# Kernel optimization log

Measured on AMD Instinct MI355X. Metric: run time of the kernel, lower is better.

The kernel has to match this reference:

```python
import jax, jax.numpy as jnp
import numpy as np


def setup_inputs() -> dict:
    key = jax.random.key(0)
    kx, ky = jax.random.split(key)
    N, D = 8192, 128
    x = jax.random.normal(kx, (N, D), dtype=jnp.float32)
    y = jax.random.normal(ky, (N, D), dtype=jnp.float32)
    return {"x": x, "y": y}


def reference(x, y):
    # L2 contrastive loss (Kostic et al. 2024, NCP):
    #   1/(N(N-1)) * sum_{i != j} <x_i, y_j>^2  -  2/N * sum_i <x_i, y_i>
    N = x.shape[0]
    K = x @ y.T                      # (N, N) pairwise dot products
    diag = jnp.diagonal(K)           # <x_i, y_i>
    off_diag_sq = jnp.sum(K * K) - jnp.sum(diag * diag)
    loss = off_diag_sq / (N * (N - 1)) - 2.0 / N * jnp.sum(diag)
    return loss
```

## Files before the change

kernel.cpp:

```cpp
#include <hip/hip_runtime.h>

#define DD 128
#define SR 72
#define PP 128
#define NB (2*PP)
#define NT 36
#define DOTB 144

typedef float f32x4 __attribute__((ext_vector_type(4)));
typedef short s16x8 __attribute__((ext_vector_type(8)));

__global__ __launch_bounds__(512)
void gram_kernel(const float* __restrict__ x, const float* __restrict__ y,
                 float* __restrict__ apart, float* __restrict__ bpart,
                 double* __restrict__ ds1, double* __restrict__ ds2,
                 float* __restrict__ out, int N)
{
  const int blk = blockIdx.x;
  const bool isX = blk < PP;
  const int p = isX ? blk : blk - PP;
  const float* __restrict__ src = isX ? x : y;
  const int slab = N / PP;
  const int row0 = p * slab;

  __shared__ __align__(16) unsigned short sh_hi[DD * SR];
  __shared__ __align__(16) unsigned short sh_lo[DD * SR];
  __shared__ double wred[8][2];

  const int tid = threadIdx.x;
  const int wave = tid >> 6, lane = tid & 63;
  const int rloc = tid >> 3;
  const int fg = tid & 7;

  if (blk == 0 && tid == 0) out[0] = 0.0f;

  const int start = (9 * wave) >> 1;
  const int cnt = 4 + (wave & 1);
  int tr_[5], tc_[5];
#pragma unroll
  for (int j = 0; j < 5; ++j) {
    const int tile = start + j;
    int r = 0;
#pragma unroll
    for (int q = 1; q < 8; ++q) r += (tile >= ((q * (17 - q)) >> 1)) ? 1 : 0;
    tr_[j] = r;
    tc_[j] = tile - ((r * (17 - r)) >> 1) + r;
  }

  f32x4 acc[5];
#pragma unroll
  for (int t = 0; t < 5; ++t)
#pragma unroll
    for (int k = 0; k < 4; ++k) acc[t][k] = 0.f;

  double s1 = 0.0, s2 = 0.0;

  {
    const float* cb = src + (size_t)row0 * DD;
    const float4* rowp = (const float4*)(cb + rloc * DD);
    float4 v0 = rowp[fg], v1 = rowp[fg + 8], v2 = rowp[fg + 16], v3 = rowp[fg + 24];

    if (isX) {
      const float4* yrp = (const float4*)(y + (size_t)row0 * DD + rloc * DD);
      float4 w0 = yrp[fg], w1 = yrp[fg + 8], w2 = yrp[fg + 16], w3 = yrp[fg + 24];
      float d = v0.x*w0.x + v0.y*w0.y + v0.z*w0.z + v0.w*w0.w
              + v1.x*w1.x + v1.y*w1.y + v1.z*w1.z + v1.w*w1.w
              + v2.x*w2.x + v2.y*w2.y + v2.z*w2.z + v2.w*w2.w
              + v3.x*w3.x + v3.y*w3.y + v3.z*w3.z + v3.w*w3.w;
      d += __shfl_down(d, 4, 8);
      d += __shfl_down(d, 2, 8);
      d += __shfl_down(d, 1, 8);
      if (fg == 0) { s1 += (double)d; s2 += (double)d * (double)d; }
    }

    {
      float vals[16] = {v0.x, v0.y, v0.z, v0.w, v1.x, v1.y, v1.z, v1.w,
                        v2.x, v2.y, v2.z, v2.w, v3.x, v3.y, v3.z, v3.w};
#pragma unroll
      for (int j = 0; j < 4; ++j)
#pragma unroll
        for (int cc = 0; cc < 4; ++cc) {
          const int m = ((fg + (j << 3)) << 2) + cc;
          const float vv = vals[j * 4 + cc];
          const unsigned int b = __float_as_uint(vv);
          const unsigned short hb = (unsigned short)(b >> 16);
          const float hf = __uint_as_float(b & 0xffff0000u);
          const float lf = vv - hf;
          const unsigned short lb = (unsigned short)(__float_as_uint(lf) >> 16);
          sh_hi[m * SR + rloc] = hb;
          sh_lo[m * SR + rloc] = lb;
        }
    }
    __syncthreads();

#pragma unroll
    for (int j = 0; j < 5; ++j) {
      if (j < cnt) {
        const int ar0 = (tr_[j] * 16 + (lane & 15)) * SR;
        const int br0 = (tc_[j] * 16 + (lane & 15)) * SR;
#pragma unroll
        for (int kb = 0; kb < 64; kb += 32) {
          const int ko = kb + ((lane >> 4) << 3);
          const s16x8 ahi = *(const s16x8*)&sh_hi[ar0 + ko];
          const s16x8 alo = *(const s16x8*)&sh_lo[ar0 + ko];
          const s16x8 bhi = *(const s16x8*)&sh_hi[br0 + ko];
          const s16x8 blo = *(const s16x8*)&sh_lo[br0 + ko];
          acc[j] = __builtin_amdgcn_mfma_f32_16x16x32_bf16(ahi, bhi, acc[j], 0, 0, 0);
          acc[j] = __builtin_amdgcn_mfma_f32_16x16x32_bf16(ahi, blo, acc[j], 0, 0, 0);
          acc[j] = __builtin_amdgcn_mfma_f32_16x16x32_bf16(alo, bhi, acc[j], 0, 0, 0);
        }
      }
    }
  }

  f32x4* __restrict__ dst4 = (f32x4*)(isX ? apart : bpart) + (size_t)p * (NT * 64);
#pragma unroll
  for (int j = 0; j < 5; ++j)
    if (j < cnt) dst4[(start + j) * 64 + lane] = acc[j];

  if (isX) {
    s1 += __shfl_down(s1, 32, 64); s2 += __shfl_down(s2, 32, 64);
    s1 += __shfl_down(s1, 16, 64); s2 += __shfl_down(s2, 16, 64);
    s1 += __shfl_down(s1, 8, 64);  s2 += __shfl_down(s2, 8, 64);
    if (lane == 0) { wred[wave][0] = s1; wred[wave][1] = s2; }
    __syncthreads();
    if (tid == 0) {
      double t1 = 0.0, t2 = 0.0;
#pragma unroll
      for (int g = 0; g < 8; ++g) { t1 += wred[g][0]; t2 += wred[g][1]; }
      ds1[p] = t1;
      ds2[p] = t2;
    }
  }
}

__global__ __launch_bounds__(256)
void dotfin_kernel(const float* __restrict__ apart, const float* __restrict__ bpart,
                   const double* __restrict__ ds1, const double* __restrict__ ds2,
                   float* __restrict__ out, int N)
{
  __shared__ f32x4 sA[16][16], sB[16][16];
  __shared__ double red[4][2];

  const int blk = blockIdx.x;
  const int tid = threadIdx.x;
  const double invNN1 = 1.0 / ((double)N * (double)(N - 1));

  if (blk < DOTB) {
    const int s = tid & 15;
    const int pg = tid >> 4;
    const f32x4* a4 = (const f32x4*)apart;
    const f32x4* b4 = (const f32x4*)bpart;
    const int base = blk * 16 + s;

    f32x4 sa = {0.f, 0.f, 0.f, 0.f}, sb = {0.f, 0.f, 0.f, 0.f};
#pragma unroll
    for (int i = 0; i < 8; ++i) {
      const int p = pg + (i << 4);
      sa += a4[(size_t)p * (NT * 64) + base];
      sb += b4[(size_t)p * (NT * 64) + base];
    }

    sA[pg][s] = sa;
    sB[pg][s] = sb;
    __syncthreads();

    if (tid < 16) {
      f32x4 ta = sA[0][tid], tb = sB[0][tid];
#pragma unroll
      for (int g = 1; g < 16; ++g) { ta += sA[g][tid]; tb += sB[g][tid]; }
      const int tile = (blk * 16 + tid) >> 6;
      const double w = ((0xA44208101ULL >> tile) & 1) ? 1.0 : 2.0;
      double pr = w * ((double)ta[0] * (double)tb[0]
                     + (double)ta[1] * (double)tb[1]
                     + (double)ta[2] * (double)tb[2]
                     + (double)ta[3] * (double)tb[3]);
      pr += __shfl_down(pr, 8, 16);
      pr += __shfl_down(pr, 4, 16);
      pr += __shfl_down(pr, 2, 16);
      pr += __shfl_down(pr, 1, 16);
      if (tid == 0) atomicAdd(out, (float)(pr * invNN1));
    }
  } else {
    const int wv = tid >> 6, lane = tid & 63;
    double t1 = (tid < PP) ? ds1[tid] : 0.0;
    double t2 = (tid < PP) ? ds2[tid] : 0.0;
#pragma unroll
    for (int off = 32; off > 0; off >>= 1) {
      t1 += __shfl_down(t1, off, 64);
      t2 += __shfl_down(t2, off, 64);
    }
    if (lane == 0) { red[wv][0] = t1; red[wv][1] = t2; }
    __syncthreads();
    if (tid == 0) {
      double d1 = red[0][0] + red[1][0] + red[2][0] + red[3][0];
      double d2 = red[0][1] + red[1][1] + red[2][1] + red[3][1];
      atomicAdd(out, (float)(-d2 * invNN1 - (2.0 / N) * d1));
    }
  }
}

extern "C" void kernel_launch(void* const* d_in, const int* in_sizes, int n_in,
                              void* d_out, int out_size, void* d_ws, size_t ws_size,
                              hipStream_t stream) {
  const float* x = (const float*)d_in[0];
  const float* y = (const float*)d_in[1];
  float* out = (float*)d_out;
  const int N = in_sizes[0] / DD;

  char* w = (char*)d_ws;
  float* apart = (float*)w;                              w += (size_t)PP * NT * 256 * 4;
  float* bpart = (float*)w;                              w += (size_t)PP * NT * 256 * 4;
  double* ds1  = (double*)w;                             w += PP * 8;
  double* ds2  = (double*)w;                             w += PP * 8;

  gram_kernel<<<NB, 512, 0, stream>>>(x, y, apart, bpart, ds1, ds2, out, N);
  dotfin_kernel<<<DOTB + 1, 256, 0, stream>>>(apart, bpart, ds1, ds2, out, N);
}
```

Before: 68.81 us.

## Split Gram tile work across twice as many blocks and widen finalize grid

The gram kernel now launches 512 blocks instead of 256. Each slab's 36 upper-triangular 16x16 Gram tiles are split into two halves of 18, and each block computes only one half. This gives each wave 2-3 tiles instead of 4-5 and improves CU coverage on a 256-CU part. The cost is that every slab is loaded and split into bf16 hi/lo twice. The dot/finalize kernel doubles its block count, with each block handling 8 float4 lanes over 32 partition groups to shorten the per-block reduction.

```diff
diff --git a/kernel.cpp b/kernel.cpp
--- a/kernel.cpp
+++ b/kernel.cpp
@@ -3,9 +3,9 @@
 #define DD 128
 #define SR 72
 #define PP 128
-#define NB (2*PP)
+#define GB 512
 #define NT 36
-#define DOTB 144
+#define DOTB 288
 
 typedef float f32x4 __attribute__((ext_vector_type(4)));
 typedef short s16x8 __attribute__((ext_vector_type(8)));
@@ -16,12 +16,15 @@
                  double* __restrict__ ds1, double* __restrict__ ds2,
                  float* __restrict__ out, int N)
 {
-  const int blk = blockIdx.x;
-  const bool isX = blk < PP;
-  const int p = isX ? blk : blk - PP;
+  const int b = blockIdx.x;
+  const int half = b >> 8;
+  const int inner = b & 255;
+  const bool isX = inner < PP;
+  const int p = inner & (PP - 1);
   const float* __restrict__ src = isX ? x : y;
   const int slab = N / PP;
   const int row0 = p * slab;
+  const bool doDiag = isX && (half == 0);
 
   __shared__ __align__(16) unsigned short sh_hi[DD * SR];
   __shared__ __align__(16) unsigned short sh_lo[DD * SR];
@@ -32,14 +35,14 @@
   const int rloc = tid >> 3;
   const int fg = tid & 7;
 
-  if (blk == 0 && tid == 0) out[0] = 0.0f;
-
-  const int start = (9 * wave) >> 1;
-  const int cnt = 4 + (wave & 1);
-  int tr_[5], tc_[5];
-#pragma unroll
-  for (int j = 0; j < 5; ++j) {
-    const int tile = start + j;
+  if (b == 0 && tid == 0) out[0] = 0.0f;
+
+  const int start = 2 * wave + (wave == 7 ? 1 : 0);
+  const int cnt = (wave >= 6) ? 3 : 2;
+  int tr_[3], tc_[3];
+#pragma unroll
+  for (int j = 0; j < 3; ++j) {
+    const int tile = 18 * half + start + j;
     int r = 0;
 #pragma unroll
     for (int q = 1; q < 8; ++q) r += (tile >= ((q * (17 - q)) >> 1)) ? 1 : 0;
@@ -47,9 +50,9 @@
     tc_[j] = tile - ((r * (17 - r)) >> 1) + r;
   }
 
-  f32x4 acc[5];
-#pragma unroll
-  for (int t = 0; t < 5; ++t)
+  f32x4 acc[3];
+#pragma unroll
+  for (int t = 0; t < 3; ++t)
 #pragma unroll
     for (int k = 0; k < 4; ++k) acc[t][k] = 0.f;
 
@@ -60,7 +63,7 @@
     const float4* rowp = (const float4*)(cb + rloc * DD);
     float4 v0 = rowp[fg], v1 = rowp[fg + 8], v2 = rowp[fg + 16], v3 = rowp[fg + 24];
 
-    if (isX) {
+    if (doDiag) {
       const float4* yrp = (const float4*)(y + (size_t)row0 * DD + rloc * DD);
       float4 w0 = yrp[fg], w1 = yrp[fg + 8], w2 = yrp[fg + 16], w3 = yrp[fg + 24];
       float d = v0.x*w0.x + v0.y*w0.y + v0.z*w0.z + v0.w*w0.w
@@ -82,9 +85,9 @@
         for (int cc = 0; cc < 4; ++cc) {
           const int m = ((fg + (j << 3)) << 2) + cc;
           const float vv = vals[j * 4 + cc];
-          const unsigned int b = __float_as_uint(vv);
-          const unsigned short hb = (unsigned short)(b >> 16);
-          const float hf = __uint_as_float(b & 0xffff0000u);
+          const unsigned int bb = __float_as_uint(vv);
+          const unsigned short hb = (unsigned short)(bb >> 16);
+          const float hf = __uint_as_float(bb & 0xffff0000u);
           const float lf = vv - hf;
           const unsigned short lb = (unsigned short)(__float_as_uint(lf) >> 16);
           sh_hi[m * SR + rloc] = hb;
@@ -94,7 +97,7 @@
     __syncthreads();
 
 #pragma unroll
-    for (int j = 0; j < 5; ++j) {
+    for (int j = 0; j < 3; ++j) {
       if (j < cnt) {
         const int ar0 = (tr_[j] * 16 + (lane & 15)) * SR;
         const int br0 = (tc_[j] * 16 + (lane & 15)) * SR;
@@ -115,14 +118,16 @@
 
   f32x4* __restrict__ dst4 = (f32x4*)(isX ? apart : bpart) + (size_t)p * (NT * 64);
 #pragma unroll
-  for (int j = 0; j < 5; ++j)
-    if (j < cnt) dst4[(start + j) * 64 + lane] = acc[j];
-
-  if (isX) {
+  for (int j = 0; j < 3; ++j)
+    if (j < cnt) dst4[(18 * half + start + j) * 64 + lane] = acc[j];
+
+  if (doDiag) {
     s1 += __shfl_down(s1, 32, 64); s2 += __shfl_down(s2, 32, 64);
     s1 += __shfl_down(s1, 16, 64); s2 += __shfl_down(s2, 16, 64);
     s1 += __shfl_down(s1, 8, 64);  s2 += __shfl_down(s2, 8, 64);
     if (lane == 0) { wred[wave][0] = s1; wred[wave][1] = s2; }
+  }
+  if (doDiag) {
     __syncthreads();
     if (tid == 0) {
       double t1 = 0.0, t2 = 0.0;
@@ -139,7 +144,7 @@
                    const double* __restrict__ ds1, const double* __restrict__ ds2,
                    float* __restrict__ out, int N)
 {
-  __shared__ f32x4 sA[16][16], sB[16][16];
+  __shared__ f32x4 sA[32][9], sB[32][9];
   __shared__ double red[4][2];
 
   const int blk = blockIdx.x;
@@ -147,16 +152,16 @@
   const double invNN1 = 1.0 / ((double)N * (double)(N - 1));
 
   if (blk < DOTB) {
-    const int s = tid & 15;
-    const int pg = tid >> 4;
+    const int s = tid & 7;
+    const int pg = tid >> 3;
     const f32x4* a4 = (const f32x4*)apart;
     const f32x4* b4 = (const f32x4*)bpart;
-    const int base = blk * 16 + s;
+    const int base = blk * 8 + s;
 
     f32x4 sa = {0.f, 0.f, 0.f, 0.f}, sb = {0.f, 0.f, 0.f, 0.f};
 #pragma unroll
-    for (int i = 0; i < 8; ++i) {
-      const int p = pg + (i << 4);
+    for (int i = 0; i < 4; ++i) {
+      const int p = pg + (i << 5);
       sa += a4[(size_t)p * (NT * 64) + base];
       sb += b4[(size_t)p * (NT * 64) + base];
     }
@@ -165,20 +170,19 @@
     sB[pg][s] = sb;
     __syncthreads();
 
-    if (tid < 16) {
+    if (tid < 8) {
       f32x4 ta = sA[0][tid], tb = sB[0][tid];
 #pragma unroll
-      for (int g = 1; g < 16; ++g) { ta += sA[g][tid]; tb += sB[g][tid]; }
-      const int tile = (blk * 16 + tid) >> 6;
+      for (int g = 1; g < 32; ++g) { ta += sA[g][tid]; tb += sB[g][tid]; }
+      const int tile = (blk * 8 + tid) >> 6;
       const double w = ((0xA44208101ULL >> tile) & 1) ? 1.0 : 2.0;
       double pr = w * ((double)ta[0] * (double)tb[0]
                      + (double)ta[1] * (double)tb[1]
                      + (double)ta[2] * (double)tb[2]
                      + (double)ta[3] * (double)tb[3]);
-      pr += __shfl_down(pr, 8, 16);
-      pr += __shfl_down(pr, 4, 16);
-      pr += __shfl_down(pr, 2, 16);
-      pr += __shfl_down(pr, 1, 16);
+      pr += __shfl_down(pr, 4, 8);
+      pr += __shfl_down(pr, 2, 8);
+      pr += __shfl_down(pr, 1, 8);
       if (tid == 0) atomicAdd(out, (float)(pr * invNN1));
     }
   } else {
@@ -214,6 +218,6 @@
   double* ds1  = (double*)w;                             w += PP * 8;
   double* ds2  = (double*)w;                             w += PP * 8;
 
-  gram_kernel<<<NB, 512, 0, stream>>>(x, y, apart, bpart, ds1, ds2, out, N);
+  gram_kernel<<<GB, 512, 0, stream>>>(x, y, apart, bpart, ds1, ds2, out, N);
   dotfin_kernel<<<DOTB + 1, 256, 0, stream>>>(apart, bpart, ds1, ds2, out, N);
 }
```

New measurement: 70.68 us. +2.7%, slower.
